# Kernel optimization log

Measured on AMD Instinct MI355X. Metric: run time of the kernel, lower is better.

Reference implementation:

```python
import jax, jax.numpy as jnp
import numpy as np

NUM_EMBEDDINGS = 8192
EMBEDDING_DIM = 256
COMMITMENT_COST = 0.25


def setup_inputs() -> dict:
    key = jax.random.key(0)
    k1, k2 = jax.random.split(key)
    z = jax.random.normal(k1, (32, EMBEDDING_DIM, 32, 32), dtype=jnp.float32)
    embedding = jax.random.normal(k2, (EMBEDDING_DIM, NUM_EMBEDDINGS), dtype=jnp.float32)
    return {"z": z, "embedding": embedding}


def reference(z, embedding):
    # z: [B, D, H, W]; embedding: [D, K]
    B, D, H, W = z.shape
    z_perm = jnp.transpose(z, (0, 2, 3, 1))          # [B, H, W, D]
    flat_z = z_perm.reshape(-1, D)                    # [N, D]
    # squared euclidean distances: ||z||^2 - 2 z.e + ||e||^2  -> [N, K]
    distances = (
        jnp.sum(flat_z * flat_z, axis=1, keepdims=True)
        - 2.0 * (flat_z @ embedding)
        + jnp.sum(embedding * embedding, axis=0, keepdims=True)
    )
    encoding_indices = jnp.argmin(distances, axis=1)  # [N]
    # gather codebook rows (same math as one-hot @ embedding.T)
    quantized = jnp.take(embedding.T, encoding_indices, axis=0)  # [N, D]
    quantized = quantized.reshape(z_perm.shape)       # [B, H, W, D]
    quantized = jnp.transpose(quantized, (0, 3, 1, 2))  # [B, D, H, W]

    e_latent_loss = jnp.mean((jax.lax.stop_gradient(quantized) - z) ** 2)
    q_latent_loss = jnp.mean((quantized - jax.lax.stop_gradient(z)) ** 2)
    loss = q_latent_loss + COMMITMENT_COST * e_latent_loss

    # straight-through estimator
    quantized_st = z + jax.lax.stop_gradient(quantized - z)
    return quantized_st, loss
```

## Files before the change

kernel.cpp:

```cpp
#include <hip/hip_runtime.h>

typedef unsigned int u32;
typedef unsigned short u16;
typedef __attribute__((ext_vector_type(8))) short bf16x8;
typedef __attribute__((ext_vector_type(4))) float f32x4;

#define KN 8192
#define DD 256
#define HW 1024
#define NP 32768
#define SPLITS 2
#define KSPLIT 4096
#define PXT 128
#define NTT 128

__device__ __forceinline__ u16 rne_bf16(float x) {
    u32 u = __float_as_uint(x);
    return (u16)((u + 0x7FFF + ((u >> 16) & 1)) >> 16);
}

__device__ __forceinline__ void glds16(const void* g, void* ldsbase) {
    __builtin_amdgcn_global_load_lds((const __attribute__((address_space(1))) u32*)g,
                                     (__attribute__((address_space(3))) u32*)ldsbase, 16, 0, 0);
}

__global__ void enorm_kernel(const float* __restrict__ e, float* __restrict__ e2f) {
    int k = blockIdx.x * blockDim.x + threadIdx.x;
    float acc = 0.f;
#pragma unroll 8
    for (int d = 0; d < DD; ++d) {
        float v = e[(size_t)d * KN + k];
        acc = fmaf(v, v, acc);
    }
    e2f[k] = acc;
}

__global__ void prep_eT_kernel(const float* __restrict__ e, u16* __restrict__ eT,
                               float* __restrict__ eTf) {
    __shared__ float tt[64][65];
    const int t = threadIdx.x;
    const int kt = blockIdx.x;
    const int dt = blockIdx.y;
    const float* ep = e + (size_t)(dt * 64) * KN + kt * 64;
    {
        int k = t & 63, d0 = t >> 6;
#pragma unroll
        for (int j = 0; j < 16; ++j) tt[d0 + j * 4][k] = ep[(size_t)(d0 + j * 4) * KN + k];
    }
    __syncthreads();
    int k = t >> 2, c0 = (t & 3) * 16;
    u16 hi[16];
    float fv[16];
#pragma unroll
    for (int j = 0; j < 16; ++j) {
        float v = tt[c0 + j][k];
        fv[j] = v;
        hi[j] = rne_bf16(v);
    }
    u16* rowp = eT + (size_t)(kt * 64 + k) * 256 + dt * 64 + c0;
    *(uint4*)(rowp) = *(uint4*)(hi);
    *(uint4*)(rowp + 8) = *(uint4*)(hi + 8);
    float* rowpf = eTf + (size_t)(kt * 64 + k) * 256 + dt * 64 + c0;
#pragma unroll
    for (int j = 0; j < 4; ++j) *(float4*)(rowpf + j * 4) = *(float4*)(fv + j * 4);
}

__global__ void prep_A_kernel(const float* __restrict__ z, u16* __restrict__ A) {
    __shared__ float tt[64][65];
    const int t = threadIdx.x;
    const int pt = blockIdx.x;
    const int dt = blockIdx.y;
    const int b  = blockIdx.z;
    const float* zp = z + (size_t)b * (DD * HW) + (size_t)(dt * 64) * HW + pt * 64;
    {
        int p = t & 63, d0 = t >> 6;
#pragma unroll
        for (int j = 0; j < 16; ++j) tt[d0 + j * 4][p] = zp[(size_t)(d0 + j * 4) * HW + p];
    }
    __syncthreads();
    int p = t >> 2, c0 = (t & 3) * 16;
    int n = b * HW + pt * 64 + p;
    u16 hi[16];
#pragma unroll
    for (int j = 0; j < 16; ++j) hi[j] = rne_bf16(tt[c0 + j][p]);
    u16* rowp = A + (size_t)n * 256 + dt * 64 + c0;
    *(uint4*)(rowp) = *(uint4*)(hi);
    *(uint4*)(rowp + 8) = *(uint4*)(hi + 8);
}

__launch_bounds__(256, 2)
__global__ void argmin_mfma_kernel(const u16* __restrict__ A,
                                   const u16* __restrict__ eT,
                                   const float* __restrict__ e2f,
                                   int* __restrict__ keys) {
    __shared__ u16 Ast[4][PXT * 64];
    __shared__ u16 Bst[NTT * 64];

    const int t = threadIdx.x;
    const int w = t >> 6;
    const int l = t & 63;
    const int split = blockIdx.x & 1;
    const int pxt   = blockIdx.x >> 1;
    const int px0 = pxt * PXT;
    const int kb0 = split * KSPLIT;

    const int swz  = (l & 7) ^ ((l >> 3) & 7);
    const int srow = l >> 3;
    const int fr = l & 15;
    const int g  = l >> 4;

#pragma unroll
    for (int c = 0; c < 4; ++c)
#pragma unroll
        for (int i = 0; i < 4; ++i) {
            int r0 = w * 32 + i * 8;
            const u16* gp = A + (size_t)(px0 + r0 + srow) * 256 + c * 64 + swz * 8;
            glds16(gp, &Ast[c][r0 * 64]);
        }

    int b1[8], b2[8];
#pragma unroll
    for (int i = 0; i < 8; ++i) { b1[i] = 0x7FFFFFFF; b2[i] = 0x7FFFFFFF; }

    for (int nt = 0; nt < KSPLIT / NTT; ++nt) {
        const int n0 = kb0 + nt * NTT;
        f32x4 acc[2][8];
#pragma unroll
        for (int mi = 0; mi < 2; ++mi)
#pragma unroll
            for (int ni = 0; ni < 8; ++ni) acc[mi][ni] = (f32x4){0.f, 0.f, 0.f, 0.f};

        for (int kit = 0; kit < 4; ++kit) {
            __syncthreads();
#pragma unroll
            for (int i = 0; i < 4; ++i) {
                int r0 = w * 32 + i * 8;
                const u16* gp = eT + (size_t)(n0 + r0 + srow) * 256 + kit * 64 + swz * 8;
                glds16(gp, &Bst[r0 * 64]);
            }
            __syncthreads();
#pragma unroll
            for (int kc = 0; kc < 2; ++kc) {
                bf16x8 af[2], bfr[8];
#pragma unroll
                for (int mi = 0; mi < 2; ++mi) {
                    int row = w * 32 + mi * 16 + fr;
                    int slt = (kc * 4 + g) ^ (row & 7);
                    af[mi] = *(const bf16x8*)&Ast[kit][row * 64 + slt * 8];
                }
#pragma unroll
                for (int ni = 0; ni < 8; ++ni) {
                    int row = ni * 16 + fr;
                    int slt = (kc * 4 + g) ^ (row & 7);
                    bfr[ni] = *(const bf16x8*)&Bst[row * 64 + slt * 8];
                }
#pragma unroll
                for (int mi = 0; mi < 2; ++mi)
#pragma unroll
                    for (int ni = 0; ni < 8; ++ni)
                        acc[mi][ni] = __builtin_amdgcn_mfma_f32_16x16x32_bf16(
                            af[mi], bfr[ni], acc[mi][ni], 0, 0, 0);
            }
        }

        float e2c[8];
        int   kc8[8];
#pragma unroll
        for (int ni = 0; ni < 8; ++ni) {
            kc8[ni] = n0 + ni * 16 + fr;
            e2c[ni] = e2f[kc8[ni]] * 256.f;
        }
#pragma unroll
        for (int mi = 0; mi < 2; ++mi)
#pragma unroll
            for (int r = 0; r < 4; ++r) {
                int ky[8];
#pragma unroll
                for (int ni = 0; ni < 8; ++ni) {
                    float d = fmaf(acc[mi][ni][r], -512.f, e2c[ni]);
                    ky[ni] = (int)d * 8192 + kc8[ni];
                }
                int m0 = min(min(ky[0], ky[1]), ky[2]);
                int m1 = min(min(ky[3], ky[4]), ky[5]);
                int m2 = min(min(ky[6], ky[7]), m0);
                int kmin = min(m1, m2);
                int i8 = mi * 4 + r;
                int v1 = min(b1[i8], kmin);
                int x  = max(b1[i8], kmin);
                b2[i8] = min(b2[i8], x);
                b1[i8] = v1;
            }
    }

    if (true) {
        int* k1 = keys + split * NP;
        int* k2 = keys + (2 + split) * NP;
        int* k3 = keys + (4 + split) * NP;
#pragma unroll
        for (int i = 0; i < 8; ++i) {
            int c1 = b1[i], c2 = b2[i], c3 = 0x7FFFFFFF;
#pragma unroll
            for (int m = 1; m < 16; m <<= 1) {
                int a1 = __shfl_xor(c1, m, 64);
                int a2 = __shfl_xor(c2, m, 64);
                int a3 = __shfl_xor(c3, m, 64);
                int m1 = min(c1, a1);
                int xx = max(c1, a1);
                int mn2 = min(c2, a2);
                int m2 = min(xx, mn2);
                int m3 = min(min(max(c2, a2), max(xx, mn2)), min(c3, a3));
                c1 = m1; c2 = m2; c3 = m3;
            }
            if (fr == 0) {
                int mi = i >> 2, r = i & 3;
                int row = px0 + w * 32 + mi * 16 + g * 4 + r;
                k1[row] = c1;
                k2[row] = c2;
                k3[row] = c3;
            }
        }
    }
}

__global__ void combine_kernel(const int* __restrict__ keys,
                               const float* __restrict__ z,
                               const float* __restrict__ eTf,
                               const float* __restrict__ e2f,
                               int* __restrict__ idx) {
    __shared__ float zt[DD * 65];
    __shared__ int   kc[384];
    __shared__ float dval[384];
    const int t = threadIdx.x;
    const int n0 = blockIdx.x * 64;
    const float* zp = z + (size_t)(n0 >> 10) * (DD * HW) + (n0 & (HW - 1));
    for (int i = t; i < DD * 64; i += 256) {
        int d = i >> 6, p = i & 63;
        zt[d * 65 + p] = zp[(size_t)d * HW + p];
    }
    for (int i = t; i < 384; i += 256)
        kc[i] = keys[(i % 6) * NP + n0 + i / 6] & 8191;
    __syncthreads();

    const int l = t & 63, w = t >> 6;
    const int j = l & 15;
    const int s = l >> 4;
#pragma unroll 2
    for (int it = 0; it < 24; ++it) {
        int dot = it * 16 + w * 4 + s;
        int p = dot / 6, c = dot - p * 6;
        (void)c;
        int k = kc[dot];
        const float* er = eTf + (size_t)k * 256;
        float a = 0.f;
#pragma unroll
        for (int cc = 0; cc < 16; ++cc)
            a = fmaf(zt[(cc * 16 + j) * 65 + p], er[cc * 16 + j], a);
        a += __shfl_xor(a, 1, 64);
        a += __shfl_xor(a, 2, 64);
        a += __shfl_xor(a, 4, 64);
        a += __shfl_xor(a, 8, 64);
        if (j == 0) dval[dot] = fmaf(-2.f, a, e2f[k]);
    }
    __syncthreads();
    if (t < 64) {
        float bv = dval[t * 6];
        int   bk = kc[t * 6];
#pragma unroll
        for (int c = 1; c < 6; ++c) {
            float dv = dval[t * 6 + c];
            int   kk = kc[t * 6 + c];
            if (dv < bv || (dv == bv && kk < bk)) { bv = dv; bk = kk; }
        }
        idx[n0 + t] = bk;
    }
}

__global__ void gather_fast_kernel(const float* __restrict__ z,
                                   const float* __restrict__ eTf,
                                   const int* __restrict__ idx,
                                   float* __restrict__ out,
                                   float* __restrict__ loss) {
    __shared__ float qt[64 * 257];
    __shared__ int kidx[64];
    const int t = threadIdx.x;
    const int n0 = blockIdx.x * 64;
    if (t < 64) kidx[t] = idx[n0 + t];
    __syncthreads();
    for (int m = 0; m < 64; ++m)
        qt[m * 257 + t] = eTf[(size_t)kidx[m] * 256 + t];
    __syncthreads();

    const int p = t & 63, q = t >> 6;
    const size_t base = (size_t)(n0 >> 10) * (DD * HW) + (n0 & (HW - 1)) + p;
    float acc = 0.f;
#pragma unroll 8
    for (int i = 0; i < 64; ++i) {
        int d = q * 64 + i;
        float ev = qt[p * 257 + d];
        float zv = z[base + (size_t)d * HW];
        out[base + (size_t)d * HW] = zv + (ev - zv);
        float df = ev - zv;
        acc = fmaf(df, df, acc);
    }
#pragma unroll
    for (int off = 32; off > 0; off >>= 1) acc += __shfl_down(acc, off, 64);
    __shared__ float part[4];
    if ((t & 63) == 0) part[t >> 6] = acc;
    __syncthreads();
    if (t == 0) {
        float s = (part[0] + part[1] + part[2] + part[3]) * (1.25f / 8388608.f);
        atomicAdd(loss, s);
    }
}

__global__ void gather_slow_kernel(const float* __restrict__ z,
                                   const float* __restrict__ e,
                                   const int* __restrict__ idx,
                                   float* __restrict__ out,
                                   float* __restrict__ loss) {
    const int t = threadIdx.x;
    const int n0 = blockIdx.x * 64;
    __shared__ int kidx[64];
    if (t < 64) kidx[t] = idx[n0 + t];
    __syncthreads();

    const int p = t & 63;
    const int d0 = t >> 6;
    const size_t base = (size_t)(n0 >> 10) * (DD * HW) + (n0 & (HW - 1)) + p;
    const int kk = kidx[p];

    float acc = 0.f;
    for (int d = d0; d < DD; d += 4) {
        float ev = e[(size_t)d * KN + kk];
        float zv = z[base + (size_t)d * HW];
        out[base + (size_t)d * HW] = zv + (ev - zv);
        float df = ev - zv;
        acc = fmaf(df, df, acc);
    }
#pragma unroll
    for (int off = 32; off > 0; off >>= 1) acc += __shfl_down(acc, off, 64);
    __shared__ float part[4];
    if ((t & 63) == 0) part[t >> 6] = acc;
    __syncthreads();
    if (t == 0) {
        float s = (part[0] + part[1] + part[2] + part[3]) * (1.25f / 8388608.f);
        atomicAdd(loss, s);
    }
}

extern "C" void kernel_launch(void* const* d_in, const int* in_sizes, int n_in,
                              void* d_out, int out_size, void* d_ws, size_t ws_size,
                              hipStream_t stream) {
    const float* z = (const float*)d_in[0];
    const float* e = (const float*)d_in[1];
    float* out = (float*)d_out;
    float* loss = out + (size_t)NP * DD;

    char* ob = (char*)d_out;
    char* ws = (char*)d_ws;
    u16* Acat = (u16*)ob;
    u16* eT   = (u16*)(ob + ((size_t)16 << 20));

    float* e2f = (float*)ws;
    int*   idx = (int*)(ws + (32 << 10));
    int*   keys;
    float* eTf;
    const bool fastws = ws_size >= ((size_t)10 << 20);
    if (fastws) {
        keys = (int*)(ws + (160 << 10));
        eTf  = (float*)(ws + ((size_t)1 << 20));
    } else {
        keys = (int*)(ob + ((size_t)20 << 20));
        eTf  = (float*)(ob + ((size_t)23 << 20));
    }

    enorm_kernel<<<KN / 256, 256, 0, stream>>>(e, e2f);
    prep_eT_kernel<<<dim3(128, 4), 256, 0, stream>>>(e, eT, eTf);
    prep_A_kernel<<<dim3(16, 4, 32), 256, 0, stream>>>(z, Acat);
    argmin_mfma_kernel<<<SPLITS * (NP / PXT), 256, 0, stream>>>(Acat, eT, e2f, keys);
    combine_kernel<<<NP / 64, 256, 0, stream>>>(keys, z, eTf, e2f, idx);
    hipMemsetAsync(loss, 0, sizeof(float), stream);
    if (fastws)
        gather_fast_kernel<<<NP / 64, 256, 0, stream>>>(z, eTf, idx, out, loss);
    else
        gather_slow_kernel<<<NP / 64, 256, 0, stream>>>(z, e, idx, out, loss);
}
```

Baseline: 281.7 us.

## Merge prep kernels into one launch and fuse combine with gather

```diff
diff --git a/kernel.cpp b/kernel.cpp
--- a/kernel.cpp
+++ b/kernel.cpp
@@ -24,68 +24,69 @@
                                      (__attribute__((address_space(3))) u32*)ldsbase, 16, 0, 0);
 }
 
-__global__ void enorm_kernel(const float* __restrict__ e, float* __restrict__ e2f) {
-    int k = blockIdx.x * blockDim.x + threadIdx.x;
-    float acc = 0.f;
+__global__ void prep_kernel(const float* __restrict__ e, const float* __restrict__ z,
+                            u16* __restrict__ eT, float* __restrict__ eTf,
+                            float* __restrict__ e2f, u16* __restrict__ A) {
+    const int t = threadIdx.x;
+    const int bid = blockIdx.x;
+    if (bid < 32) {
+        int k = bid * 256 + t;
+        float acc = 0.f;
 #pragma unroll 8
-    for (int d = 0; d < DD; ++d) {
-        float v = e[(size_t)d * KN + k];
-        acc = fmaf(v, v, acc);
-    }
-    e2f[k] = acc;
-}
-
-__global__ void prep_eT_kernel(const float* __restrict__ e, u16* __restrict__ eT,
-                               float* __restrict__ eTf) {
-    __shared__ float tt[64][65];
-    const int t = threadIdx.x;
-    const int kt = blockIdx.x;
-    const int dt = blockIdx.y;
-    const float* ep = e + (size_t)(dt * 64) * KN + kt * 64;
-    {
-        int k = t & 63, d0 = t >> 6;
-#pragma unroll
-        for (int j = 0; j < 16; ++j) tt[d0 + j * 4][k] = ep[(size_t)(d0 + j * 4) * KN + k];
-    }
-    __syncthreads();
-    int k = t >> 2, c0 = (t & 3) * 16;
-    u16 hi[16];
-    float fv[16];
-#pragma unroll
-    for (int j = 0; j < 16; ++j) {
-        float v = tt[c0 + j][k];
-        fv[j] = v;
-        hi[j] = rne_bf16(v);
-    }
-    u16* rowp = eT + (size_t)(kt * 64 + k) * 256 + dt * 64 + c0;
-    *(uint4*)(rowp) = *(uint4*)(hi);
-    *(uint4*)(rowp + 8) = *(uint4*)(hi + 8);
-    float* rowpf = eTf + (size_t)(kt * 64 + k) * 256 + dt * 64 + c0;
-#pragma unroll
-    for (int j = 0; j < 4; ++j) *(float4*)(rowpf + j * 4) = *(float4*)(fv + j * 4);
-}
-
-__global__ void prep_A_kernel(const float* __restrict__ z, u16* __restrict__ A) {
-    __shared__ float tt[64][65];
-    const int t = threadIdx.x;
-    const int pt = blockIdx.x;
-    const int dt = blockIdx.y;
-    const int b  = blockIdx.z;
-    const float* zp = z + (size_t)b * (DD * HW) + (size_t)(dt * 64) * HW + pt * 64;
-    {
-        int p = t & 63, d0 = t >> 6;
-#pragma unroll
-        for (int j = 0; j < 16; ++j) tt[d0 + j * 4][p] = zp[(size_t)(d0 + j * 4) * HW + p];
-    }
-    __syncthreads();
-    int p = t >> 2, c0 = (t & 3) * 16;
-    int n = b * HW + pt * 64 + p;
-    u16 hi[16];
-#pragma unroll
-    for (int j = 0; j < 16; ++j) hi[j] = rne_bf16(tt[c0 + j][p]);
-    u16* rowp = A + (size_t)n * 256 + dt * 64 + c0;
-    *(uint4*)(rowp) = *(uint4*)(hi);
-    *(uint4*)(rowp + 8) = *(uint4*)(hi + 8);
+        for (int d = 0; d < DD; ++d) {
+            float v = e[(size_t)d * KN + k];
+            acc = fmaf(v, v, acc);
+        }
+        e2f[k] = acc;
+    } else if (bid < 544) {
+        __shared__ float tt[64][65];
+        const int b2 = bid - 32;
+        const int kt = b2 & 127;
+        const int dt = b2 >> 7;
+        const float* ep = e + (size_t)(dt * 64) * KN + kt * 64;
+        {
+            int k = t & 63, d0 = t >> 6;
+#pragma unroll
+            for (int j = 0; j < 16; ++j) tt[d0 + j * 4][k] = ep[(size_t)(d0 + j * 4) * KN + k];
+        }
+        __syncthreads();
+        int k = t >> 2, c0 = (t & 3) * 16;
+        u16 hi[16];
+        float fv[16];
+#pragma unroll
+        for (int j = 0; j < 16; ++j) {
+            float v = tt[c0 + j][k];
+            fv[j] = v;
+            hi[j] = rne_bf16(v);
+        }
+        u16* rowp = eT + (size_t)(kt * 64 + k) * 256 + dt * 64 + c0;
+        *(uint4*)(rowp) = *(uint4*)(hi);
+        *(uint4*)(rowp + 8) = *(uint4*)(hi + 8);
+        float* rowpf = eTf + (size_t)(kt * 64 + k) * 256 + dt * 64 + c0;
+#pragma unroll
+        for (int j = 0; j < 4; ++j) *(float4*)(rowpf + j * 4) = *(float4*)(fv + j * 4);
+    } else {
+        __shared__ float tt[64][65];
+        const int b3 = bid - 544;
+        const int pt = b3 & 15;
+        const int dt = (b3 >> 4) & 3;
+        const int b  = b3 >> 6;
+        const float* zp = z + (size_t)b * (DD * HW) + (size_t)(dt * 64) * HW + pt * 64;
+        {
+            int p = t & 63, d0 = t >> 6;
+#pragma unroll
+            for (int j = 0; j < 16; ++j) tt[d0 + j * 4][p] = zp[(size_t)(d0 + j * 4) * HW + p];
+        }
+        __syncthreads();
+        int p = t >> 2, c0 = (t & 3) * 16;
+        int n = b * HW + pt * 64 + p;
+        u16 hi[16];
+#pragma unroll
+        for (int j = 0; j < 16; ++j) hi[j] = rne_bf16(tt[c0 + j][p]);
+        u16* rowp = A + (size_t)n * 256 + dt * 64 + c0;
+        *(uint4*)(rowp) = *(uint4*)(hi);
+        *(uint4*)(rowp + 8) = *(uint4*)(hi + 8);
+    }
 }
 
 __launch_bounds__(256, 2)
@@ -192,7 +193,7 @@
             }
     }
 
-    if (true) {
+    {
         int* k1 = keys + split * NP;
         int* k2 = keys + (2 + split) * NP;
         int* k3 = keys + (4 + split) * NP;
@@ -222,6 +223,89 @@
     }
 }
 
+__global__ void finalize_kernel(const int* __restrict__ keys,
+                                const float* __restrict__ z,
+                                const float* __restrict__ eTf,
+                                const float* __restrict__ e2f,
+                                float* __restrict__ out,
+                                float* __restrict__ loss) {
+    __shared__ float smem[DD * 65];
+    __shared__ int   kc[384];
+    __shared__ float dval[384];
+    __shared__ int   kidx[64];
+    const int t = threadIdx.x;
+    const int n0 = blockIdx.x * 64;
+    const float* zp = z + (size_t)(n0 >> 10) * (DD * HW) + (n0 & (HW - 1));
+
+    for (int i = t; i < DD * 64; i += 256) {
+        int d = i >> 6, p = i & 63;
+        smem[d * 65 + p] = zp[(size_t)d * HW + p];
+    }
+    for (int i = t; i < 384; i += 256)
+        kc[i] = keys[(i % 6) * NP + n0 + i / 6] & 8191;
+    __syncthreads();
+
+    const int l = t & 63, w = t >> 6;
+    const int j = l & 15;
+    const int s = l >> 4;
+#pragma unroll 2
+    for (int it = 0; it < 24; ++it) {
+        int dot = it * 16 + w * 4 + s;
+        int p = dot / 6;
+        int k = kc[dot];
+        const float* er = eTf + (size_t)k * 256;
+        float a = 0.f;
+#pragma unroll
+        for (int cc = 0; cc < 16; ++cc)
+            a = fmaf(smem[(cc * 16 + j) * 65 + p], er[cc * 16 + j], a);
+        a += __shfl_xor(a, 1, 64);
+        a += __shfl_xor(a, 2, 64);
+        a += __shfl_xor(a, 4, 64);
+        a += __shfl_xor(a, 8, 64);
+        if (j == 0) dval[dot] = fmaf(-2.f, a, e2f[k]);
+    }
+    __syncthreads();
+    if (t < 64) {
+        float bv = dval[t * 6];
+        int   bk = kc[t * 6];
+#pragma unroll
+        for (int c = 1; c < 6; ++c) {
+            float dv = dval[t * 6 + c];
+            int   kk = kc[t * 6 + c];
+            if (dv < bv || (dv == bv && kk < bk)) { bv = dv; bk = kk; }
+        }
+        kidx[t] = bk;
+    }
+    __syncthreads();
+
+    float* qt = smem;
+    for (int m = 0; m < 64; ++m)
+        qt[m * 257 + t] = eTf[(size_t)kidx[m] * 256 + t];
+    __syncthreads();
+
+    const int p = t & 63, q = t >> 6;
+    const size_t base = (size_t)(n0 >> 10) * (DD * HW) + (n0 & (HW - 1)) + p;
+    float acc = 0.f;
+#pragma unroll 8
+    for (int i = 0; i < 64; ++i) {
+        int d = q * 64 + i;
+        float ev = qt[p * 257 + d];
+        float zv = z[base + (size_t)d * HW];
+        out[base + (size_t)d * HW] = zv + (ev - zv);
+        float df = ev - zv;
+        acc = fmaf(df, df, acc);
+    }
+#pragma unroll
+    for (int off = 32; off > 0; off >>= 1) acc += __shfl_down(acc, off, 64);
+    __shared__ float part[4];
+    if ((t & 63) == 0) part[t >> 6] = acc;
+    __syncthreads();
+    if (t == 0) {
+        float s2 = (part[0] + part[1] + part[2] + part[3]) * (1.25f / 8388608.f);
+        atomicAdd(loss, s2);
+    }
+}
+
 __global__ void combine_kernel(const int* __restrict__ keys,
                                const float* __restrict__ z,
                                const float* __restrict__ eTf,
@@ -247,8 +331,7 @@
 #pragma unroll 2
     for (int it = 0; it < 24; ++it) {
         int dot = it * 16 + w * 4 + s;
-        int p = dot / 6, c = dot - p * 6;
-        (void)c;
+        int p = dot / 6;
         int k = kc[dot];
         const float* er = eTf + (size_t)k * 256;
         float a = 0.f;
@@ -272,44 +355,6 @@
             if (dv < bv || (dv == bv && kk < bk)) { bv = dv; bk = kk; }
         }
         idx[n0 + t] = bk;
-    }
-}
-
-__global__ void gather_fast_kernel(const float* __restrict__ z,
-                                   const float* __restrict__ eTf,
-                                   const int* __restrict__ idx,
-                                   float* __restrict__ out,
-                                   float* __restrict__ loss) {
-    __shared__ float qt[64 * 257];
-    __shared__ int kidx[64];
-    const int t = threadIdx.x;
-    const int n0 = blockIdx.x * 64;
-    if (t < 64) kidx[t] = idx[n0 + t];
-    __syncthreads();
-    for (int m = 0; m < 64; ++m)
-        qt[m * 257 + t] = eTf[(size_t)kidx[m] * 256 + t];
-    __syncthreads();
-
-    const int p = t & 63, q = t >> 6;
-    const size_t base = (size_t)(n0 >> 10) * (DD * HW) + (n0 & (HW - 1)) + p;
-    float acc = 0.f;
-#pragma unroll 8
-    for (int i = 0; i < 64; ++i) {
-        int d = q * 64 + i;
-        float ev = qt[p * 257 + d];
-        float zv = z[base + (size_t)d * HW];
-        out[base + (size_t)d * HW] = zv + (ev - zv);
-        float df = ev - zv;
-        acc = fmaf(df, df, acc);
-    }
-#pragma unroll
-    for (int off = 32; off > 0; off >>= 1) acc += __shfl_down(acc, off, 64);
-    __shared__ float part[4];
-    if ((t & 63) == 0) part[t >> 6] = acc;
-    __syncthreads();
-    if (t == 0) {
-        float s = (part[0] + part[1] + part[2] + part[3]) * (1.25f / 8388608.f);
-        atomicAdd(loss, s);
     }
 }
 
@@ -374,14 +419,13 @@
         eTf  = (float*)(ob + ((size_t)23 << 20));
     }
 
-    enorm_kernel<<<KN / 256, 256, 0, stream>>>(e, e2f);
-    prep_eT_kernel<<<dim3(128, 4), 256, 0, stream>>>(e, eT, eTf);
-    prep_A_kernel<<<dim3(16, 4, 32), 256, 0, stream>>>(z, Acat);
+    prep_kernel<<<2592, 256, 0, stream>>>(e, z, eT, eTf, e2f, Acat);
     argmin_mfma_kernel<<<SPLITS * (NP / PXT), 256, 0, stream>>>(Acat, eT, e2f, keys);
-    combine_kernel<<<NP / 64, 256, 0, stream>>>(keys, z, eTf, e2f, idx);
     hipMemsetAsync(loss, 0, sizeof(float), stream);
-    if (fastws)
-        gather_fast_kernel<<<NP / 64, 256, 0, stream>>>(z, eTf, idx, out, loss);
-    else
+    if (fastws) {
+        finalize_kernel<<<NP / 64, 256, 0, stream>>>(keys, z, eTf, e2f, out, loss);
+    } else {
+        combine_kernel<<<NP / 64, 256, 0, stream>>>(keys, z, eTf, e2f, idx);
         gather_slow_kernel<<<NP / 64, 256, 0, stream>>>(z, e, idx, out, loss);
-}
+    }
+}
```

Result: faster. 267.8 us (-4.9%).
